# Optimization experiments

Measured on AMD Instinct MI355X. Metric: run time of the kernel, lower is better.

## Reference

```python
import jax, jax.numpy as jnp
import numpy as np

D_MODEL = 2048
N_HEADS = 16
D_KEY = D_MODEL // N_HEADS
ALIBI_SLOPE = 8.0
KEY_SCALE = D_KEY ** -0.5
B, S = 2, 2048


def setup_inputs() -> dict:
    key = jax.random.key(0)
    ks = jax.random.split(key, 12)
    sd = D_MODEL ** -0.5
    return {
        "states": jax.random.normal(ks[0], (B, S, D_MODEL), jnp.float32),
        "bias_mask": jax.random.normal(ks[1], (B, S, S), jnp.float32),
        # weights stored [in, out] (torch Linear applies x @ W.T + b)
        "wq": jax.random.normal(ks[2], (D_MODEL, D_MODEL), jnp.float32) * sd,
        "bq": jnp.zeros((D_MODEL,), jnp.float32),
        "wk": jax.random.normal(ks[3], (D_MODEL, D_MODEL), jnp.float32) * sd,
        "bk": jnp.zeros((D_MODEL,), jnp.float32),
        "wv": jax.random.normal(ks[4], (D_MODEL, D_MODEL), jnp.float32) * sd,
        "bv": jnp.zeros((D_MODEL,), jnp.float32),
        "wg": jax.random.normal(ks[5], (D_MODEL, N_HEADS), jnp.float32) * sd,
        "bg": jnp.zeros((N_HEADS,), jnp.float32),
        "wo": jax.random.normal(ks[6], (D_MODEL, D_MODEL), jnp.float32) * sd,
        "bo": jnp.zeros((D_MODEL,), jnp.float32),
    }


def reference(states, bias_mask, wq, bq, wk, bk, wv, bv, wg, bg, wo, bo):
    # head_scale = exp2(-(h+1)*alibi_slope/n_heads), non-trainable buffer
    head_scale = jnp.exp2(-(jnp.arange(N_HEADS, dtype=jnp.float32) + 1.0)
                          * ALIBI_SLOPE / N_HEADS)
    # [B, H, Q, K] bias with per-head ALiBi scaling
    bias = bias_mask[:, None, :, :] * head_scale[None, :, None, None]

    def heads(x, w, b):  # [B,S,D] -> [B,H,S,Dk]
        y = x @ w + b
        return y.reshape(x.shape[0], x.shape[1], N_HEADS, D_KEY).transpose(0, 2, 1, 3)

    q = heads(states, wq, bq)
    k = heads(states, wk, bk)
    v = heads(states, wv, bv)

    scores = jnp.einsum('bhqd,bhkd->bhqk', q, k) * KEY_SCALE + bias
    probs = jax.nn.softmax(scores, axis=-1)
    o = jnp.einsum('bhqk,bhkd->bqhd', probs, v)  # [B,S,H,Dk]

    g = jax.nn.sigmoid(states @ wg + bg)  # [B,S,H] head gate
    o = o * g[..., None]

    return o.reshape(o.shape[0], o.shape[1], D_MODEL) @ wo + bo
```

## Files before the change

### kernel.cpp

```cpp
#include <hip/hip_runtime.h>
#include <hip/hip_bf16.h>

#define SEQ 2048
#define DM 2048
#define NH 16
#define DK 128
#define LOG2E 1.4426950408889634f
#define QK_SCALE 0.08838834764831845f

typedef __attribute__((ext_vector_type(8))) short short8;
typedef __attribute__((ext_vector_type(4))) float f32x4;
typedef __attribute__((ext_vector_type(4))) unsigned short us4;

__device__ __forceinline__ unsigned short f2b(float f) {
  union { float f; unsigned u; } v; v.f = f;
  unsigned r = v.u + 0x7fffu + ((v.u >> 16) & 1u);
  return (unsigned short)(r >> 16);
}
__device__ __forceinline__ float b2f(unsigned short v) {
  union { unsigned u; float f; } x; x.u = ((unsigned)v) << 16; return x.f;
}

__device__ __forceinline__ void gl_lds16(const void* g, void* l) {
  __builtin_amdgcn_global_load_lds((const __attribute__((address_space(1))) void*)g,
                                   (__attribute__((address_space(3))) void*)l, 16, 0, 0);
}

#define SBAR()   __builtin_amdgcn_s_barrier()
#define SCHED0() __builtin_amdgcn_sched_barrier(0)
#define LGKM0()  asm volatile("s_waitcnt lgkmcnt(0)" ::: "memory")

__global__ __launch_bounds__(256) void cast2_bf16_kernel(const float* __restrict__ in0,
                                                         unsigned short* __restrict__ out0,
                                                         const float* __restrict__ in1,
                                                         unsigned short* __restrict__ out1) {
  int bid = blockIdx.x;
  const float* in = (bid < 4096) ? in0 : in1;
  unsigned short* out = (bid < 4096) ? out0 : out1;
  int i = ((bid < 4096) ? bid : bid - 4096) * 256 + threadIdx.x;
  const float4* p = (const float4*)in;
  float4 a = p[2*i], b = p[2*i+1];
  us4 r0, r1;
  r0[0]=f2b(a.x); r0[1]=f2b(a.y); r0[2]=f2b(a.z); r0[3]=f2b(a.w);
  r1[0]=f2b(b.x); r1[1]=f2b(b.y); r1[2]=f2b(b.z); r1[3]=f2b(b.w);
  us4* o = (us4*)out;
  o[2*i] = r0; o[2*i+1] = r1;
}

__global__ __launch_bounds__(256) void transpose_cast4_kernel(const float* __restrict__ w0,
                                                              const float* __restrict__ w1,
                                                              const float* __restrict__ w2,
                                                              const float* __restrict__ w3,
                                                              unsigned short* __restrict__ dst) {
  const float* w = (blockIdx.z == 0) ? w0 : (blockIdx.z == 1) ? w1 : (blockIdx.z == 2) ? w2 : w3;
  unsigned short* wt = dst + (size_t)blockIdx.z * DM * DM;
  __shared__ float t[64][65];
  int c0 = blockIdx.x * 64, r0 = blockIdx.y * 64;
  int tid = threadIdx.x;
  int rr = tid >> 4;
  int c4 = (tid & 15) * 4;
#pragma unroll
  for (int p = 0; p < 4; ++p) {
    int r = p*16 + rr;
    float4 v = *(const float4*)&w[(size_t)(r0 + r)*DM + c0 + c4];
    t[r][c4] = v.x; t[r][c4+1] = v.y; t[r][c4+2] = v.z; t[r][c4+3] = v.w;
  }
  __syncthreads();
#pragma unroll
  for (int p = 0; p < 4; ++p) {
    int c = p*16 + rr;
    us4 v;
    v[0] = f2b(t[c4+0][c]); v[1] = f2b(t[c4+1][c]);
    v[2] = f2b(t[c4+2][c]); v[3] = f2b(t[c4+3][c]);
    *(us4*)&wt[(size_t)(c0 + c)*DM + r0 + c4] = v;
  }
}

__global__ __launch_bounds__(256) void transpose_wg_kernel(const float* __restrict__ wg,
                                                           unsigned short* __restrict__ wgT) {
  int idx = blockIdx.x * 256 + threadIdx.x;
  int c = idx & 15;
  int r0 = (idx >> 4) * 4;
#pragma unroll
  for (int r = 0; r < 4; ++r)
    wgT[(size_t)c*DM + r0 + r] = f2b(wg[(size_t)(r0 + r)*NH + c]);
}

__device__ __forceinline__ void gemm128_core(const unsigned short* __restrict__ A,
                                             const unsigned short* __restrict__ Bt,
                                             int m0, int n0, f32x4 (&acc)[4][4]) {
  __shared__ __align__(16) unsigned short Ab[2][8192];
  __shared__ __align__(16) unsigned short Bb[2][2][8192];
  const int TK = DM / 64;

  int tid = threadIdx.x, wid = tid >> 6, lane = tid & 63;
  int lo = lane & 15, hi = lane >> 4;
  int wm = wid >> 2, wn = wid & 3;
  int w2 = wid * 2;

  int srow8 = lane >> 3;
  int skb = (((lane & 7) ^ srow8) << 4);
  const char* Ag = (const char*)A;
  const char* Bg = (const char*)Bt;

#define STG_A(S,CUR) do {                                                          \
    const char* g = Ag + (size_t)(S)*128 + skb;                                    \
    char* l = (char*)&Ab[CUR][0] + w2*1024;                                        \
    gl_lds16(g + (size_t)(m0 + w2*8 + srow8)*4096,     l);                         \
    gl_lds16(g + (size_t)(m0 + w2*8 + 8 + srow8)*4096, l + 1024);                  \
  } while(0)
#define STG_B(S,CUR) do {                                                          \
    const char* g = Bg + (size_t)(S)*128 + skb;                                    \
    char* l = (char*)&Bb[CUR][0][0] + w2*1024;                                     \
    gl_lds16(g + (size_t)(n0 + w2*8 + srow8)*4096,           l);                   \
    gl_lds16(g + (size_t)(n0 + w2*8 + 8 + srow8)*4096,       l + 1024);            \
    gl_lds16(g + (size_t)(n0 + 128 + w2*8 + srow8)*4096,     l + 16384);           \
    gl_lds16(g + (size_t)(n0 + 128 + w2*8 + 8 + srow8)*4096, l + 16384 + 1024);    \
  } while(0)

#pragma unroll
  for (int i = 0; i < 4; ++i)
#pragma unroll
    for (int j = 0; j < 4; ++j) acc[i][j] = (f32x4){0.f,0.f,0.f,0.f};

  STG_B(0,0); STG_A(0,0); STG_B(1,1); STG_A(1,1);
  asm volatile("s_waitcnt vmcnt(6)" ::: "memory");
  SBAR();

  int msk = (lo & 7) << 4;
  int k0 = (hi*16) ^ msk;
  int k1 = (64 + hi*16) ^ msk;
  int brow = (wn & 1) * 64;

  short8 a[4][2], bA[2][2], bB[2][2];

#define MF16(NHH,BF)                                                                \
  __builtin_amdgcn_s_setprio(1);                                                    \
  _Pragma("unroll") for (int mi = 0; mi < 4; ++mi)                                  \
  _Pragma("unroll") for (int nn = 0; nn < 2; ++nn) {                                \
    acc[mi][(NHH)*2+nn] = __builtin_amdgcn_mfma_f32_16x16x32_bf16(                  \
        a[mi][0], BF[nn][0], acc[mi][(NHH)*2+nn], 0, 0, 0);                         \
    acc[mi][(NHH)*2+nn] = __builtin_amdgcn_mfma_f32_16x16x32_bf16(                  \
        a[mi][1], BF[nn][1], acc[mi][(NHH)*2+nn], 0, 0, 0);                         \
  }                                                                                 \
  __builtin_amdgcn_s_setprio(0);

  for (int s = 0; s < TK; ++s) {
    int cur = s & 1;
    const char* Ac = (const char*)&Ab[cur][0];
    const char* Bc = (const char*)&Bb[cur][wn >> 1][0];
    bool pre = (s + 2) < TK;

#pragma unroll
    for (int mm = 0; mm < 4; ++mm) {
      a[mm][0] = *(const short8*)(Ac + (wm*64 + mm*16 + lo)*128 + k0);
      a[mm][1] = *(const short8*)(Ac + (wm*64 + mm*16 + lo)*128 + k1);
    }
#pragma unroll
    for (int nn = 0; nn < 2; ++nn) {
      bA[nn][0] = *(const short8*)(Bc + (brow + nn*16 + lo)*128 + k0);
      bA[nn][1] = *(const short8*)(Bc + (brow + nn*16 + lo)*128 + k1);
      bB[nn][0] = *(const short8*)(Bc + (brow + (2+nn)*16 + lo)*128 + k0);
      bB[nn][1] = *(const short8*)(Bc + (brow + (2+nn)*16 + lo)*128 + k1);
    }
    SBAR(); LGKM0(); SCHED0();
    MF16(0, bA);
    SBAR();

    if (pre) {
      STG_B(s + 2, cur);
      STG_A(s + 2, cur);
      asm volatile("s_waitcnt vmcnt(6)" ::: "memory");
    } else if (s == TK - 2) {
      asm volatile("s_waitcnt vmcnt(0)" ::: "memory");
    }
    SBAR();
    MF16(1, bB);
    SBAR();
  }
#undef STG_A
#undef STG_B
#undef MF16
}

__global__ __launch_bounds__(512, 2) void gemm128_qkv_kernel(const unsigned short* __restrict__ A,
                                                             const unsigned short* __restrict__ Bt,
                                                             const float* __restrict__ bq,
                                                             const float* __restrict__ bk,
                                                             const float* __restrict__ bv,
                                                             unsigned short* __restrict__ QB,
                                                             unsigned short* __restrict__ KB,
                                                             unsigned short* __restrict__ VTB) {
  f32x4 acc[4][4];
  int n0 = blockIdx.x * 256, m0 = blockIdx.y * 128;
  gemm128_core(A, Bt, m0, n0, acc);

  int tid = threadIdx.x, wid = tid >> 6, lane = tid & 63;
  int lo = lane & 15, hi = lane >> 4;
  int wm = wid >> 2, wn = wid & 3;
  int m_base = m0 + wm*64;
  int n_base = n0 + wn*64;
  int sect = n0 >> 11;

  if (sect == 2) {
#pragma unroll
    for (int mi = 0; mi < 4; ++mi) {
      int m = m_base + mi*16 + 4*hi;
      int b = m >> 11, srow = m & 2047;
#pragma unroll
      for (int nf = 0; nf < 4; ++nf) {
        int n = n_base + nf*16 + lo;
        int nl = n & 2047, h = nl >> 7, d = nl & 127;
        float bvv = bv[nl];
        us4 pk;
#pragma unroll
        for (int r = 0; r < 4; ++r) pk[r] = f2b(acc[mi][nf][r] + bvv);
        *(us4*)&VTB[(((size_t)(b*NH + h))*DK + d)*SEQ + srow] = pk;
      }
    }
  } else {
    unsigned short* out = sect ? KB : QB;
    const float* bp = sect ? bk : bq;
    const float qs = sect ? 1.f : QK_SCALE * LOG2E;
#pragma unroll
    for (int mi = 0; mi < 4; ++mi) {
#pragma unroll
      for (int nf = 0; nf < 4; ++nf) {
        int n = n_base + nf*16 + lo;
        int nl = n & 2047, h = nl >> 7, d = nl & 127;
        float bvv = bp[nl];
#pragma unroll
        for (int r = 0; r < 4; ++r) {
          int m = m_base + mi*16 + 4*hi + r;
          int b = m >> 11, srow = m & 2047;
          out[(((size_t)(b*NH + h))*SEQ + srow)*DK + d] = f2b((acc[mi][nf][r] + bvv) * qs);
        }
      }
    }
  }
}

__global__ __launch_bounds__(512, 2) void gemm128_ao_kernel(const unsigned short* __restrict__ A,
                                                            const unsigned short* __restrict__ Bt,
                                                            const float* __restrict__ bias,
                                                            float* __restrict__ out) {
  f32x4 acc[4][4];
  int n0 = blockIdx.x * 256, m0 = blockIdx.y * 128;
  gemm128_core(A, Bt, m0, n0, acc);

  int tid = threadIdx.x, wid = tid >> 6, lane = tid & 63;
  int lo = lane & 15, hi = lane >> 4;
  int wm = wid >> 2, wn = wid & 3;
#pragma unroll
  for (int mi = 0; mi < 4; ++mi) {
#pragma unroll
    for (int nf = 0; nf < 4; ++nf) {
      int n = n0 + wn*64 + nf*16 + lo;
      float bvv = bias[n];
#pragma unroll
      for (int r = 0; r < 4; ++r) {
        int m = m0 + wm*64 + mi*16 + 4*hi + r;
        out[(size_t)m*DM + n] = acc[mi][nf][r] + bvv;
      }
    }
  }
}

__global__ __launch_bounds__(256) void gate_mfma_kernel(const unsigned short* __restrict__ XB,
                                                        const unsigned short* __restrict__ wgT,
                                                        const float* __restrict__ bg,
                                                        float* __restrict__ G) {
  int tid = threadIdx.x, wid = tid >> 6, lane = tid & 63;
  int lo = lane & 15, hi = lane >> 4;
  int m0 = blockIdx.x * 64 + wid * 16;

  f32x4 acc = {0.f, 0.f, 0.f, 0.f};
  const unsigned short* xrow = XB + (size_t)(m0 + lo) * DM + hi * 8;
  const unsigned short* grow = wgT + (size_t)lo * DM + hi * 8;
#pragma unroll 4
  for (int kt = 0; kt < DM; kt += 32) {
    short8 a = *(const short8*)(xrow + kt);
    short8 b = *(const short8*)(grow + kt);
    acc = __builtin_amdgcn_mfma_f32_16x16x32_bf16(a, b, acc, 0, 0, 0);
  }
  float bgv = bg[lo];
#pragma unroll
  for (int r = 0; r < 4; ++r) {
    float x = acc[r] + bgv;
    G[(size_t)(m0 + 4*hi + r) * NH + lo] = 1.f / (1.f + __builtin_amdgcn_exp2f(-x * LOG2E));
  }
}

__global__ __attribute__((amdgpu_flat_work_group_size(512,512)))
__attribute__((amdgpu_waves_per_eu(2,4)))
void attn_kernel(const unsigned short* __restrict__ Q,
                 const unsigned short* __restrict__ Kb,
                 const unsigned short* __restrict__ VT,
                 const unsigned short* __restrict__ biasb,
                 const float* __restrict__ G,
                 unsigned short* __restrict__ OG) {
  __shared__ __align__(16) unsigned short kbuf[2][64*128];
  __shared__ __align__(16) unsigned short vbuf[2][128*64];
  __shared__ __align__(16) unsigned short pbuf[8*16*64];

  int bid = blockIdx.x;
  int h  = bid & 15;
  int b  = (bid >> 4) & 1;
  int qt = bid >> 5;
  int bh = b*NH + h;

  int tid = threadIdx.x, wid = tid >> 6, lane = tid & 63;
  int lo = lane & 15, hi = lane >> 4;
  int qw0 = qt*256 + wid*32;

  float hs2 = __builtin_amdgcn_exp2f(-(float)(h+1) * 0.5f) * LOG2E;

  short8 qf[2][4];
#pragma unroll
  for (int f2 = 0; f2 < 2; ++f2)
#pragma unroll
    for (int ks = 0; ks < 4; ++ks)
      qf[f2][ks] = *(const short8*)&Q[((size_t)bh*SEQ + qw0 + f2*16 + lo)*DK + ks*32 + hi*8];

  f32x4 zero4 = {0.f,0.f,0.f,0.f};
  f32x4 acco[2][8];
#pragma unroll
  for (int f2 = 0; f2 < 2; ++f2)
#pragma unroll
    for (int f = 0; f < 8; ++f) acco[f2][f] = zero4;
  float lrun[2][4];
#pragma unroll
  for (int f2 = 0; f2 < 2; ++f2)
#pragma unroll
    for (int r = 0; r < 4; ++r) lrun[f2][r] = 0.f;

  const char* kbase = (const char*)Kb + ((size_t)bh*SEQ)*DK*2;
  const char* vbase = (const char*)VT + ((size_t)bh*DK)*SEQ*2;
  const unsigned short* bb = biasb + ((size_t)b*SEQ + qw0 + 4*hi)*SEQ + lo;
  char* pb = (char*)pbuf + wid*2048;

  int s16 = lane >> 4, srow8 = lane >> 3;
  int kof = (lane & 15) * 16, vof = (lane & 7) * 16;
  int w2 = wid * 2;

#define STAGE_KV(KT, BUF) do {                                                        \
    _Pragma("unroll")                                                                 \
    for (int c = 0; c < 2; ++c) {                                                     \
      int krc = (w2 + c)*4 + s16;                                                     \
      gl_lds16(kbase + (size_t)((KT) + krc)*256 + (kof ^ ((krc & 7) << 4)),           \
               (char*)kbuf[BUF] + (w2 + c)*1024);                                     \
      int vrc = (w2 + c)*8 + srow8;                                                   \
      gl_lds16(vbase + (size_t)vrc*4096 + (size_t)(KT)*2 + (vof ^ (srow8 << 4)),      \
               (char*)vbuf[BUF] + (w2 + c)*1024);                                     \
    }                                                                                 \
  } while(0)

  unsigned short br[2][4][4];
#pragma unroll
  for (int f2 = 0; f2 < 2; ++f2)
#pragma unroll
    for (int r = 0; r < 4; ++r)
#pragma unroll
      for (int nf = 0; nf < 4; ++nf)
        br[f2][r][nf] = bb[(size_t)(f2*16 + r)*SEQ + nf*16];
  STAGE_KV(0, 0);
  STAGE_KV(64, 1);
  asm volatile("s_waitcnt vmcnt(4)" ::: "memory");
  SBAR();

  const int NT = SEQ / 64;
  int cur = 0;
  for (int t = 0; t < NT; ++t) {
#pragma unroll
    for (int f2 = 0; f2 < 2; ++f2) {
      f32x4 sf[4];
      __builtin_amdgcn_s_setprio(1);
#pragma unroll
      for (int nf = 0; nf < 4; ++nf) {
        f32x4 a = zero4;
#pragma unroll
        for (int ks = 0; ks < 4; ++ks) {
          int krw = nf*16 + lo;
          int cb = (ks*32 + hi*8)*2;
          short8 kf = *(const short8*)((const char*)kbuf[cur] + krw*256 + (cb ^ ((krw & 7) << 4)));
          a = __builtin_amdgcn_mfma_f32_16x16x32_bf16(qf[f2][ks], kf, a, 0, 0, 0);
        }
        sf[nf] = a;
      }
      __builtin_amdgcn_s_setprio(0);

#pragma unroll
      for (int r = 0; r < 4; ++r) {
        int prow = 4*hi + r;
#pragma unroll
        for (int nf = 0; nf < 4; ++nf) {
          float s = fmaf(b2f(br[f2][r][nf]), hs2, sf[nf][r]);
          float p = __builtin_amdgcn_exp2f(s);
          lrun[f2][r] += p;
          *(unsigned short*)(pb + prow*128 + ((((nf*16 + lo)*2)) ^ ((prow & 7) << 4))) = f2b(p);
        }
      }

      short8 pf[2];
#pragma unroll
      for (int ks = 0; ks < 2; ++ks)
        pf[ks] = *(const short8*)(pb + lo*128 + ((ks*64 + hi*16) ^ ((lo & 7) << 4)));
      __builtin_amdgcn_s_setprio(1);
#pragma unroll
      for (int f = 0; f < 8; ++f) {
#pragma unroll
        for (int ks = 0; ks < 2; ++ks) {
          int vrw = f*16 + lo;
          int cb = (ks*32 + hi*8)*2;
          short8 vf = *(const short8*)((const char*)vbuf[cur] + vrw*128 + (cb ^ ((vrw & 7) << 4)));
          acco[f2][f] = __builtin_amdgcn_mfma_f32_16x16x32_bf16(pf[ks], vf, acco[f2][f], 0, 0, 0);
        }
      }
      __builtin_amdgcn_s_setprio(0);
    }

    LGKM0(); SBAR();

    bool more1 = (t + 1) < NT;
    bool more2 = (t + 2) < NT;
    if (more1) {
      int ktn = (t + 1) * 64;
#pragma unroll
      for (int f2 = 0; f2 < 2; ++f2)
#pragma unroll
        for (int r = 0; r < 4; ++r)
#pragma unroll
          for (int nf = 0; nf < 4; ++nf)
            br[f2][r][nf] = bb[(size_t)(f2*16 + r)*SEQ + ktn + nf*16];
    }
    if (more2) {
      STAGE_KV((t + 2) * 64, cur);
      asm volatile("s_waitcnt vmcnt(36)" ::: "memory");
    } else if (more1) {
      asm volatile("s_waitcnt vmcnt(32)" ::: "memory");
    }
    SBAR();
    cur ^= 1;
  }
#undef STAGE_KV

#pragma unroll
  for (int f2 = 0; f2 < 2; ++f2)
#pragma unroll
    for (int r = 0; r < 4; ++r) {
      float l = lrun[f2][r];
      l += __shfl_xor(l, 1); l += __shfl_xor(l, 2);
      l += __shfl_xor(l, 4); l += __shfl_xor(l, 8);
      lrun[f2][r] = l;
    }

#pragma unroll
  for (int f2 = 0; f2 < 2; ++f2)
#pragma unroll
    for (int r = 0; r < 4; ++r) {
      int qrow = qw0 + f2*16 + 4*hi + r;
      float inv = 1.f / lrun[f2][r];
      float g = G[((size_t)(b*SEQ + qrow))*NH + h];
      float sgl = inv * g;
#pragma unroll
      for (int f = 0; f < 8; ++f)
        OG[((size_t)(b*SEQ) + qrow)*DM + h*DK + f*16 + lo] = f2b(acco[f2][f][r] * sgl);
    }
}

extern "C" void kernel_launch(void* const* d_in, const int* in_sizes, int n_in,
                              void* d_out, int out_size, void* d_ws, size_t ws_size,
                              hipStream_t stream) {
  const float* states    = (const float*)d_in[0];
  const float* bias_mask = (const float*)d_in[1];
  const float* wq = (const float*)d_in[2];
  const float* bq = (const float*)d_in[3];
  const float* wk = (const float*)d_in[4];
  const float* bk = (const float*)d_in[5];
  const float* wv = (const float*)d_in[6];
  const float* bv = (const float*)d_in[7];
  const float* wg = (const float*)d_in[8];
  const float* bg = (const float*)d_in[9];
  const float* wo = (const float*)d_in[10];
  const float* bo = (const float*)d_in[11];

  char* ws = (char*)d_ws;
  unsigned short* XB   = (unsigned short*)(ws + 0);
  unsigned short* OGB  = XB;
  unsigned short* WQVT = (unsigned short*)(ws + 16777216UL);
  unsigned short* WOT  = (unsigned short*)(ws + 41943040UL);
  unsigned short* QB   = (unsigned short*)(ws + 50331648UL);
  unsigned short* KB   = (unsigned short*)(ws + 67108864UL);
  unsigned short* VTB  = (unsigned short*)(ws + 83886080UL);
  unsigned short* BIASB= (unsigned short*)(ws + 100663296UL);
  float*          GB   = (float*)         (ws + 117440512UL);
  unsigned short* WGT  = (unsigned short*)(ws + 117702656UL);

  cast2_bf16_kernel<<<8192, 256, 0, stream>>>(states, XB, bias_mask, BIASB);
  transpose_cast4_kernel<<<dim3(32, 32, 4), 256, 0, stream>>>(wq, wk, wv, wo, WQVT);
  transpose_wg_kernel<<<32, 256, 0, stream>>>(wg, WGT);

  gemm128_qkv_kernel<<<dim3(24, 32), 512, 0, stream>>>(XB, WQVT, bq, bk, bv, QB, KB, VTB);

  gate_mfma_kernel<<<64, 256, 0, stream>>>(XB, WGT, bg, GB);

  attn_kernel<<<256, 512, 0, stream>>>(QB, KB, VTB, BIASB, GB, OGB);

  gemm128_ao_kernel<<<dim3(8, 32), 512, 0, stream>>>(OGB, WOT, bo, (float*)d_out);
}
```

Baseline: 333.6 us.

## Shrink projection GEMM tiles to 128x128 with 256-thread blocks

The shared GEMM core changes from a 128x256 tile computed by 8 waves to a 128x128 tile computed by 4 waves. Each wave keeps the same 64x64 output footprint and now stages four rows per call. QKV and output-projection grids double, giving more blocks, better CU fill for the small output GEMM, and less LDS per block. The cost is lower operand reuse per tile, so more global and L2 traffic for the B matrix.

```diff
diff --git a/kernel.cpp b/kernel.cpp
--- a/kernel.cpp
+++ b/kernel.cpp
@@ -86,17 +86,16 @@
     wgT[(size_t)c*DM + r0 + r] = f2b(wg[(size_t)(r0 + r)*NH + c]);
 }
 
-__device__ __forceinline__ void gemm128_core(const unsigned short* __restrict__ A,
-                                             const unsigned short* __restrict__ Bt,
-                                             int m0, int n0, f32x4 (&acc)[4][4]) {
+__device__ __forceinline__ void gemm128x128_core(const unsigned short* __restrict__ A,
+                                                 const unsigned short* __restrict__ Bt,
+                                                 int m0, int n0, f32x4 (&acc)[4][4]) {
   __shared__ __align__(16) unsigned short Ab[2][8192];
-  __shared__ __align__(16) unsigned short Bb[2][2][8192];
+  __shared__ __align__(16) unsigned short Bb[2][8192];
   const int TK = DM / 64;
 
   int tid = threadIdx.x, wid = tid >> 6, lane = tid & 63;
   int lo = lane & 15, hi = lane >> 4;
-  int wm = wid >> 2, wn = wid & 3;
-  int w2 = wid * 2;
+  int wm = wid >> 1, wn = wid & 1;
 
   int srow8 = lane >> 3;
   int skb = (((lane & 7) ^ srow8) << 4);
@@ -105,17 +104,17 @@
 
 #define STG_A(S,CUR) do {                                                          \
     const char* g = Ag + (size_t)(S)*128 + skb;                                    \
-    char* l = (char*)&Ab[CUR][0] + w2*1024;                                        \
-    gl_lds16(g + (size_t)(m0 + w2*8 + srow8)*4096,     l);                         \
-    gl_lds16(g + (size_t)(m0 + w2*8 + 8 + srow8)*4096, l + 1024);                  \
+    char* l = (char*)&Ab[CUR][0] + wid*4096;                                       \
+    _Pragma("unroll")                                                              \
+    for (int c = 0; c < 4; ++c)                                                    \
+      gl_lds16(g + (size_t)(m0 + wid*32 + c*8 + srow8)*4096, l + c*1024);          \
   } while(0)
 #define STG_B(S,CUR) do {                                                          \
     const char* g = Bg + (size_t)(S)*128 + skb;                                    \
-    char* l = (char*)&Bb[CUR][0][0] + w2*1024;                                     \
-    gl_lds16(g + (size_t)(n0 + w2*8 + srow8)*4096,           l);                   \
-    gl_lds16(g + (size_t)(n0 + w2*8 + 8 + srow8)*4096,       l + 1024);            \
-    gl_lds16(g + (size_t)(n0 + 128 + w2*8 + srow8)*4096,     l + 16384);           \
-    gl_lds16(g + (size_t)(n0 + 128 + w2*8 + 8 + srow8)*4096, l + 16384 + 1024);    \
+    char* l = (char*)&Bb[CUR][0] + wid*4096;                                       \
+    _Pragma("unroll")                                                              \
+    for (int c = 0; c < 4; ++c)                                                    \
+      gl_lds16(g + (size_t)(n0 + wid*32 + c*8 + srow8)*4096, l + c*1024);          \
   } while(0)
 
 #pragma unroll
@@ -124,13 +123,12 @@
     for (int j = 0; j < 4; ++j) acc[i][j] = (f32x4){0.f,0.f,0.f,0.f};
 
   STG_B(0,0); STG_A(0,0); STG_B(1,1); STG_A(1,1);
-  asm volatile("s_waitcnt vmcnt(6)" ::: "memory");
+  asm volatile("s_waitcnt vmcnt(8)" ::: "memory");
   SBAR();
 
   int msk = (lo & 7) << 4;
   int k0 = (hi*16) ^ msk;
   int k1 = (64 + hi*16) ^ msk;
-  int brow = (wn & 1) * 64;
 
   short8 a[4][2], bA[2][2], bB[2][2];
 
@@ -148,7 +146,7 @@
   for (int s = 0; s < TK; ++s) {
     int cur = s & 1;
     const char* Ac = (const char*)&Ab[cur][0];
-    const char* Bc = (const char*)&Bb[cur][wn >> 1][0];
+    const char* Bc = (const char*)&Bb[cur][0];
     bool pre = (s + 2) < TK;
 
 #pragma unroll
@@ -158,10 +156,10 @@
     }
 #pragma unroll
     for (int nn = 0; nn < 2; ++nn) {
-      bA[nn][0] = *(const short8*)(Bc + (brow + nn*16 + lo)*128 + k0);
-      bA[nn][1] = *(const short8*)(Bc + (brow + nn*16 + lo)*128 + k1);
-      bB[nn][0] = *(const short8*)(Bc + (brow + (2+nn)*16 + lo)*128 + k0);
-      bB[nn][1] = *(const short8*)(Bc + (brow + (2+nn)*16 + lo)*128 + k1);
+      bA[nn][0] = *(const short8*)(Bc + (wn*64 + nn*16 + lo)*128 + k0);
+      bA[nn][1] = *(const short8*)(Bc + (wn*64 + nn*16 + lo)*128 + k1);
+      bB[nn][0] = *(const short8*)(Bc + (wn*64 + (2+nn)*16 + lo)*128 + k0);
+      bB[nn][1] = *(const short8*)(Bc + (wn*64 + (2+nn)*16 + lo)*128 + k1);
     }
     SBAR(); LGKM0(); SCHED0();
     MF16(0, bA);
@@ -170,7 +168,7 @@
     if (pre) {
       STG_B(s + 2, cur);
       STG_A(s + 2, cur);
-      asm volatile("s_waitcnt vmcnt(6)" ::: "memory");
+      asm volatile("s_waitcnt vmcnt(8)" ::: "memory");
     } else if (s == TK - 2) {
       asm volatile("s_waitcnt vmcnt(0)" ::: "memory");
     }
@@ -183,7 +181,7 @@
 #undef MF16
 }
 
-__global__ __launch_bounds__(512, 2) void gemm128_qkv_kernel(const unsigned short* __restrict__ A,
+__global__ __launch_bounds__(256, 2) void gemm128_qkv_kernel(const unsigned short* __restrict__ A,
                                                              const unsigned short* __restrict__ Bt,
                                                              const float* __restrict__ bq,
                                                              const float* __restrict__ bk,
@@ -192,12 +190,12 @@
                                                              unsigned short* __restrict__ KB,
                                                              unsigned short* __restrict__ VTB) {
   f32x4 acc[4][4];
-  int n0 = blockIdx.x * 256, m0 = blockIdx.y * 128;
-  gemm128_core(A, Bt, m0, n0, acc);
+  int n0 = blockIdx.x * 128, m0 = blockIdx.y * 128;
+  gemm128x128_core(A, Bt, m0, n0, acc);
 
   int tid = threadIdx.x, wid = tid >> 6, lane = tid & 63;
   int lo = lane & 15, hi = lane >> 4;
-  int wm = wid >> 2, wn = wid & 3;
+  int wm = wid >> 1, wn = wid & 1;
   int m_base = m0 + wm*64;
   int n_base = n0 + wn*64;
   int sect = n0 >> 11;
@@ -240,17 +238,17 @@
   }
 }
 
-__global__ __launch_bounds__(512, 2) void gemm128_ao_kernel(const unsigned short* __restrict__ A,
+__global__ __launch_bounds__(256, 2) void gemm128_ao_kernel(const unsigned short* __restrict__ A,
                                                             const unsigned short* __restrict__ Bt,
                                                             const float* __restrict__ bias,
                                                             float* __restrict__ out) {
   f32x4 acc[4][4];
-  int n0 = blockIdx.x * 256, m0 = blockIdx.y * 128;
-  gemm128_core(A, Bt, m0, n0, acc);
+  int n0 = blockIdx.x * 128, m0 = blockIdx.y * 128;
+  gemm128x128_core(A, Bt, m0, n0, acc);
 
   int tid = threadIdx.x, wid = tid >> 6, lane = tid & 63;
   int lo = lane & 15, hi = lane >> 4;
-  int wm = wid >> 2, wn = wid & 3;
+  int wm = wid >> 1, wn = wid & 1;
 #pragma unroll
   for (int mi = 0; mi < 4; ++mi) {
 #pragma unroll
@@ -500,11 +498,11 @@
   transpose_cast4_kernel<<<dim3(32, 32, 4), 256, 0, stream>>>(wq, wk, wv, wo, WQVT);
   transpose_wg_kernel<<<32, 256, 0, stream>>>(wg, WGT);
 
-  gemm128_qkv_kernel<<<dim3(24, 32), 512, 0, stream>>>(XB, WQVT, bq, bk, bv, QB, KB, VTB);
+  gemm128_qkv_kernel<<<dim3(48, 32), 256, 0, stream>>>(XB, WQVT, bq, bk, bv, QB, KB, VTB);
 
   gate_mfma_kernel<<<64, 256, 0, stream>>>(XB, WGT, bg, GB);
 
   attn_kernel<<<256, 512, 0, stream>>>(QB, KB, VTB, BIASB, GB, OGB);
 
-  gemm128_ao_kernel<<<dim3(8, 32), 512, 0, stream>>>(OGB, WOT, bo, (float*)d_out);
-}
+  gemm128_ao_kernel<<<dim3(16, 32), 256, 0, stream>>>(OGB, WOT, bo, (float*)d_out);
+}
```

New measurement: 323.7 us (median of 2 runs). -3.0%, faster.
